# Kernel optimization log

Measured on AMD Instinct MI355X. Metric: run time of the kernel, lower is better.

The kernel has to match this reference:

```python
import jax, jax.numpy as jnp
import numpy as np

B, D, A, K, M = 32768, 64, 32, 16, 128


def _spec(W):
    # SpectralLinear: weight divided by its largest singular value
    s = jnp.linalg.norm(W, ord=2)
    return W / (s + 1e-6)


def setup_inputs() -> dict:
    key = jax.random.key(0)
    ks = jax.random.split(key, 20)

    def rn(i, shape):
        return jax.random.normal(ks[i], shape, jnp.float32) / np.float32(np.sqrt(shape[0]))

    return {
        "z": jax.random.normal(ks[0], (B, D), jnp.float32),
        "action": jax.random.normal(ks[1], (B, A), jnp.float32),
        "rw": jax.random.uniform(ks[2], (B, K), jnp.float32),
        "control": jax.random.normal(ks[3], (B, D), jnp.float32),
        # ActionTokenizer(action_dim, d_model, latent_dim) params (act / control / chart)
        "act_Wx": rn(4, (A + D, M)), "act_bx": jnp.zeros((M,), jnp.float32), "act_Wz": rn(5, (A, D)),
        "ctl_Wx": rn(6, (2 * D, M)), "ctl_bx": jnp.zeros((M,), jnp.float32), "ctl_Wz": rn(7, (D, D)),
        "cht_Wx": rn(8, (K + D, M)), "cht_bx": jnp.zeros((M,), jnp.float32), "cht_Wz": rn(9, (K, D)),
        # z_embed
        "We": rn(10, (D, M)), "be": jnp.zeros((M,), jnp.float32),
        # CovariantAttention (n_heads=1)
        "Wq": rn(11, (M, M)), "Wk": rn(12, (M, M)), "Wv": rn(13, (M, M)), "Wo": rn(14, (M, M)),
        # Spectral output heads
        "cons_W": rn(15, (M, 1)), "cons_b": jnp.zeros((1,), jnp.float32),
        "form_W": rn(16, (M, D)), "form_b": jnp.zeros((D,), jnp.float32),
    }


def reference(z, action, rw, control,
              act_Wx, act_bx, act_Wz,
              ctl_Wx, ctl_bx, ctl_Wz,
              cht_Wx, cht_bx, cht_Wz,
              We, be, Wq, Wk, Wv, Wo,
              cons_W, cons_b, form_W, form_b):
    def tok(u, Wx, bx, Wz):
        # tokenizer: feature token in d_model + associated latent position token
        x = jnp.tanh(jnp.concatenate([u, z], axis=-1) @ Wx + bx)   # [B, M]
        zt = z + jnp.tanh(u @ Wz)                                   # [B, D]
        return x, zt

    act_x, act_z = tok(action, act_Wx, act_bx, act_Wz)
    ctl_x, ctl_z = tok(control, ctl_Wx, ctl_bx, ctl_Wz)
    cht_x, cht_z = tok(rw, cht_Wx, cht_bx, cht_Wz)

    ctx_x = jnp.stack([act_x, ctl_x, cht_x], axis=1)  # [B, 3, M]
    ctx_z = jnp.stack([act_z, ctl_z, cht_z], axis=1)  # [B, 3, D]

    x_q = z @ We + be                                  # [B, M]

    # CovariantAttention: dot-product scores with metric-aware (geodesic distance) bias
    q = x_q @ Wq                                       # [B, M]
    k = ctx_x @ Wk                                     # [B, 3, M]
    v = ctx_x @ Wv                                     # [B, 3, M]
    dist2 = jnp.sum((z[:, None, :] - ctx_z) ** 2, axis=-1)          # [B, 3]
    scores = jnp.einsum('bm,btm->bt', q, k) / np.float32(np.sqrt(M)) - dist2
    attn = jax.nn.softmax(scores, axis=-1)             # [B, 3]
    feat = jnp.einsum('bt,btm->bm', attn, v) @ Wo      # [B, M]

    # Spectral output heads
    reward_conservative = feat @ _spec(cons_W) + cons_b            # [B, 1]
    reward_form_cov = feat @ _spec(form_W) + form_b                # [B, D]
    reward_nonconservative = jnp.sum(reward_form_cov * control, axis=-1, keepdims=True)

    return reward_conservative + reward_nonconservative            # [B, 1]
```

## Files before the change

### kernel.cpp

```cpp
#include <hip/hip_runtime.h>
#include <hip/hip_bf16.h>


typedef float f32x4 __attribute__((ext_vector_type(4)));
typedef short s16x8 __attribute__((ext_vector_type(8)));

#define OFF_ACTX  0
#define OFF_CTLX  24
#define OFF_CHTX  56
#define OFF_ACTZ  80
#define OFF_CTLZ  84
#define OFF_CHTZ  92
#define OFF_WEQK  96
#define OFF_WVOFT 112
#define N_TILES   128
#define SIG_OFF   (N_TILES*1024)
#define PREP_OFF  (SIG_OFF + 256)

__device__ __forceinline__ unsigned short f2bf(float f){
  unsigned u = __float_as_uint(f);
  u += 0x7fffu + ((u>>16)&1u);
  return (unsigned short)(u>>16);
}

__device__ __forceinline__ unsigned cvtpk(float lo, float hi){
  unsigned r;
  asm("v_cvt_pk_bf16_f32 %0, %1, %2" : "=v"(r) : "v"(lo), "v"(hi));
  return r;
}

union V8 { s16x8 v; unsigned short us[8]; uint4 q; };

__device__ __forceinline__ f32x4 MF(s16x8 a, s16x8 b, f32x4 c){
  return __builtin_amdgcn_mfma_f32_16x16x32_bf16(a, b, c, 0, 0, 0);
}

__device__ __forceinline__ s16x8 ldB(const unsigned short* pk, int tile, int lane){
  V8 t;
  t.q = *reinterpret_cast<const uint4*>(pk + ((tile<<6) + lane)*8);
  return t.v;
}

__device__ __forceinline__ s16x8 ldA_g(const float* __restrict__ p, int ko, int limit){
  V8 t;
  if (ko < limit){
    const float4* q4 = reinterpret_cast<const float4*>(p + ko);
    float4 a = q4[0], b = q4[1];
    t.q = make_uint4(cvtpk(a.x,a.y), cvtpk(a.z,a.w), cvtpk(b.x,b.y), cvtpk(b.z,b.w));
  } else {
    t.q = make_uint4(0u,0u,0u,0u);
  }
  return t.v;
}

__device__ __forceinline__ float tanh_fast(float x){
  float e = __expf(2.f*x);
  return 1.f - 2.f*__builtin_amdgcn_rcpf(e + 1.f);
}

__global__ __launch_bounds__(256) void prep_all(
    const float* __restrict__ We, const float* __restrict__ be,
    const float* __restrict__ Wq, const float* __restrict__ Wk,
    const float* __restrict__ Wv, const float* __restrict__ Wo,
    const float* __restrict__ consW, const float* __restrict__ formW,
    const float* __restrict__ aWx, const float* __restrict__ cWx,
    const float* __restrict__ hWx, const float* __restrict__ aWz,
    const float* __restrict__ cWz, const float* __restrict__ hWz,
    unsigned short* __restrict__ packed, float* __restrict__ prep,
    float* __restrict__ sig)
{
  const int b = blockIdx.x;
  const int tid = threadIdx.x;

  if (b < 130){
    __shared__ float Msh[128][129];
    __shared__ float Msh2[128][129];
    __shared__ float tsh[128];
    __shared__ float ph[2][128];
    const int half = tid >> 7, t128 = tid & 127;
    const int m0 = half*64;
    if (b <= 64){
      for (int i4 = tid; i4 < 4096; i4 += 256){
        float4 v = ((const float4*)Wk)[i4];
        int r = i4 >> 5, c = (i4 & 31) << 2;
        Msh[r][c] = v.x; Msh[r][c+1] = v.y; Msh[r][c+2] = v.z; Msh[r][c+3] = v.w;
      }
      const float* rowv = (b == 64) ? be : (We + (size_t)b*128);
      {
        float s = 0.f;
        for (int m = m0; m < m0+64; ++m) s += rowv[m]*Wq[(size_t)m*128 + t128];
        ph[half][t128] = s;
      }
      __syncthreads();
      if (tid < 128) tsh[tid] = ph[0][tid] + ph[1][tid];
      __syncthreads();
      {
        float s1 = 0.f;
        for (int p = m0; p < m0+64; ++p) s1 += tsh[p]*Msh[t128][p];
        ph[half][t128] = s1;
      }
      __syncthreads();
      if (tid < 128){
        float s1 = ph[0][tid] + ph[1][tid];
        if (b == 64) prep[16384 + tid] = s1;
        else {
          int r = b;
          int T = OFF_WEQK + ((r>>5)<<3) + (tid>>4);
          int l2 = (((r&31)>>3)<<4) | (tid&15);
          packed[((size_t)T*64 + l2)*8 + (r&7)] = f2bf(s1);
        }
      }
    } else {
      int d = b - 65;
      for (int i4 = tid; i4 < 4096; i4 += 256){
        float4 v = ((const float4*)Wo)[i4];
        int r = i4 >> 5, c = (i4 & 31) << 2;
        Msh[r][c] = v.x; Msh[r][c+1] = v.y; Msh[r][c+2] = v.z; Msh[r][c+3] = v.w;
      }
      for (int i4 = tid; i4 < 4096; i4 += 256){
        float4 v = ((const float4*)Wv)[i4];
        int r = i4 >> 5, c = (i4 & 31) << 2;
        Msh2[r][c] = v.x; Msh2[r][c+1] = v.y; Msh2[r][c+2] = v.z; Msh2[r][c+3] = v.w;
      }
      __syncthreads();
      {
        float s = 0.f;
        if (d < 64){ for (int j = m0; j < m0+64; ++j) s += Msh[t128][j]*formW[(size_t)j*64 + d]; }
        else       { for (int j = m0; j < m0+64; ++j) s += Msh[t128][j]*consW[j]; }
        ph[half][t128] = s;
      }
      __syncthreads();
      if (tid < 128) tsh[tid] = ph[0][tid] + ph[1][tid];
      __syncthreads();
      {
        float s1 = 0.f;
        for (int p = m0; p < m0+64; ++p) s1 += Msh2[t128][p]*tsh[p];
        ph[half][t128] = s1;
      }
      __syncthreads();
      if (tid < 128){
        float s1 = ph[0][tid] + ph[1][tid];
        if (d < 64){
          int r = d;
          int T = OFF_WVOFT + ((r>>5)<<3) + (tid>>4);
          int l2 = (((r&31)>>3)<<4) | (tid&15);
          packed[((size_t)T*64 + l2)*8 + (r&7)] = f2bf(s1);
        } else prep[16512 + tid] = s1;
      }
    }
    return;
  }

  if (b == 130){
    __shared__ unsigned short SW[8192];
    __shared__ unsigned short SG[4096];

    #pragma unroll
    for (int s4 = 0; s4 < 4; ++s4){
      int q = tid*4 + s4;
      int T = q >> 6, l = q & 63;
      V8 t;
      #pragma unroll
      for (int i = 0; i < 8; ++i){
        int k = (T>>2)*32 + ((l>>4)<<3) + i;
        int n = ((T&3)<<4) + (l&15);
        t.us[i] = f2bf(formW[(size_t)k*64 + n]);
      }
      *reinterpret_cast<uint4*>(&SW[q*8]) = t.q;
    }
    __syncthreads();
    if (tid >= 64) return;
    const int l = tid;
    const f32x4 z4 = {0.f,0.f,0.f,0.f};

    float cs;
    { float c0 = consW[l], c1 = consW[l+64];
      cs = c0*c0 + c1*c1;
      #pragma unroll
      for (int m = 1; m < 64; m <<= 1) cs += __shfl_xor(cs, m);
    }

    s16x8 wf[4][4];
    #pragma unroll
    for (int kt = 0; kt < 4; ++kt)
      #pragma unroll
      for (int x = 0; x < 4; ++x)
        wf[kt][x] = *reinterpret_cast<const s16x8*>(&SW[((((kt<<2)+x)<<6) | l)*8]);

    f32x4 D[4][4];
    #pragma unroll
    for (int it = 0; it < 4; ++it)
      #pragma unroll
      for (int nt = 0; nt < 4; ++nt){
        f32x4 a = z4;
        #pragma unroll
        for (int kt = 0; kt < 4; ++kt) a = MF(wf[kt][it], wf[kt][nt], a);
        D[it][nt] = a;
      }

    float L;
    {
      float ss = 0.f;
      #pragma unroll
      for (int it = 0; it < 4; ++it)
        #pragma unroll
        for (int nt = 0; nt < 4; ++nt)
          #pragma unroll
          for (int j = 0; j < 4; ++j) ss += D[it][nt][j]*D[it][nt][j];
      #pragma unroll
      for (int m = 1; m < 64; m <<= 1) ss += __shfl_xor(ss, m);
      float n0 = sqrtf(ss);
      L = logf(n0);
      float iv = 1.f/n0;
      #pragma unroll
      for (int it = 0; it < 4; ++it){
        int rb2 = it*16 + ((l>>4)<<2);
        int lp  = (((rb2&31)>>3)<<4) | (l&15);
        int ib  = rb2 & 7;
        int ktg = rb2 >> 5;
        #pragma unroll
        for (int nt = 0; nt < 4; ++nt){
          unsigned w0 = (unsigned)f2bf(D[it][nt][0]*iv) | ((unsigned)f2bf(D[it][nt][1]*iv)<<16);
          unsigned w1 = (unsigned)f2bf(D[it][nt][2]*iv) | ((unsigned)f2bf(D[it][nt][3]*iv)<<16);
          uint2 u; u.x = w0; u.y = w1;
          *reinterpret_cast<uint2*>(&SG[((((ktg<<2)+nt)<<6 | lp))*8 + ib]) = u;
        }
      }
    }

    for (int s = 1; s <= 6; ++s){
      s16x8 gf[2][4];
      #pragma unroll
      for (int kt = 0; kt < 2; ++kt)
        #pragma unroll
        for (int x = 0; x < 4; ++x)
          gf[kt][x] = *reinterpret_cast<const s16x8*>(&SG[((((kt<<2)+x)<<6) | l)*8]);
      f32x4 E[4][4];
      #pragma unroll
      for (int it = 0; it < 4; ++it)
        #pragma unroll
        for (int nt = 0; nt < 4; ++nt){
          f32x4 a = MF(gf[0][it], gf[0][nt], z4);
          E[it][nt] = MF(gf[1][it], gf[1][nt], a);
        }
      float ss = 0.f;
      #pragma unroll
      for (int it = 0; it < 4; ++it)
        #pragma unroll
        for (int nt = 0; nt < 4; ++nt)
          #pragma unroll
          for (int j = 0; j < 4; ++j) ss += E[it][nt][j]*E[it][nt][j];
      #pragma unroll
      for (int m = 1; m < 64; m <<= 1) ss += __shfl_xor(ss, m);
      float ns = sqrtf(ss);
      L = 2.f*L + logf(ns);
      if (s < 6){
        float iv = 1.f/ns;
        #pragma unroll
        for (int it = 0; it < 4; ++it){
          int rb2 = it*16 + ((l>>4)<<2);
          int lp  = (((rb2&31)>>3)<<4) | (l&15);
          int ib  = rb2 & 7;
          int ktg = rb2 >> 5;
          #pragma unroll
          for (int nt = 0; nt < 4; ++nt){
            unsigned w0 = (unsigned)f2bf(E[it][nt][0]*iv) | ((unsigned)f2bf(E[it][nt][1]*iv)<<16);
            unsigned w1 = (unsigned)f2bf(E[it][nt][2]*iv) | ((unsigned)f2bf(E[it][nt][3]*iv)<<16);
            uint2 u; u.x = w0; u.y = w1;
            *reinterpret_cast<uint2*>(&SG[((((ktg<<2)+nt)<<6 | lp))*8 + ib]) = u;
          }
        }
      }
    }

    if (l == 0){
      float sf = expf(L*(1.f/128.f));
      sig[0] = 1.f/(sf + 1e-6f);
      sig[1] = 1.f/(sqrtf(cs) + 1e-6f);
    }
    return;
  }

  {
    int tile = b - 131;
    const float* W; int N; int kind = 0; int base;
    if      (tile < 24) { W=aWx; N=128; base=OFF_ACTX; }
    else if (tile < 56) { W=cWx; N=128; base=OFF_CTLX; }
    else if (tile < 80) { W=hWx; N=128; base=OFF_CHTX; kind=1; }
    else if (tile < 84) { W=aWz; N=64;  base=OFF_ACTZ; }
    else if (tile < 92) { W=cWz; N=64;  base=OFF_CTLZ; }
    else                { W=hWz; N=64;  base=OFF_CHTZ; kind=2; }
    int NT = N >> 4;
    int lt = tile - base;
    int nt = lt % NT, kt = lt / NT;
    int l = tid >> 2, i0 = (tid & 3)*2;
    unsigned short us2[2];
    #pragma unroll
    for (int di = 0; di < 2; ++di){
      int i = i0 + di;
      int k = kt*32 + ((l>>4)<<3) + i;
      int n = nt*16 + (l & 15);
      int sr = k;
      if (kind == 1) sr = (k < 16) ? k : (k < 32 ? -1 : k - 16);
      else if (kind == 2) sr = (k < 16) ? k : -1;
      float v = (sr >= 0) ? W[(size_t)sr*N + n] : 0.f;
      us2[di] = f2bf(v);
    }
    *reinterpret_cast<unsigned*>(&packed[((size_t)tile*64 + l)*8 + i0]) =
        (unsigned)us2[0] | ((unsigned)us2[1] << 16);
  }
}

template<int KTX, int KTZ>
__device__ __forceinline__ void token_dot2(
    const unsigned short* pk, int offX, const s16x8 (*afX)[2],
    int offZ, const s16x8 (*afZ)[2], const float* __restrict__ bx,
    int lane, int ntb, int nzb,
    const f32x4 qw[2][4], const f32x4 hw[2][4],
    float st[2][4], float hs[2][4])
{
  const int r15 = lane & 15;
  const f32x4 z4 = {0.f,0.f,0.f,0.f};
  f32x4 acc[2][4];
  #pragma unroll
  for (int s = 0; s < 2; ++s)
    #pragma unroll
    for (int nl = 0; nl < 4; ++nl) acc[s][nl] = z4;
  #pragma unroll
  for (int kt = 0; kt < KTX; ++kt){
    #pragma unroll
    for (int nl = 0; nl < 4; ++nl){
      s16x8 bfr = ldB(pk, offX + kt*8 + ntb + nl, lane);
      acc[0][nl] = MF(afX[kt][0], bfr, acc[0][nl]);
      acc[1][nl] = MF(afX[kt][1], bfr, acc[1][nl]);
    }
  }
  float qs[2][4], hp[2][4];
  #pragma unroll
  for (int s = 0; s < 2; ++s)
    #pragma unroll
    for (int j = 0; j < 4; ++j){ qs[s][j] = 0.f; hp[s][j] = 0.f; }
  #pragma unroll
  for (int nl = 0; nl < 4; ++nl){
    float bv = bx[(ntb + nl)*16 + r15];
    #pragma unroll
    for (int s = 0; s < 2; ++s)
      #pragma unroll
      for (int j = 0; j < 4; ++j){
        float x = tanh_fast(acc[s][nl][j] + bv);
        qs[s][j] += x*qw[s][nl][j];
        hp[s][j] += x*hw[s][nl][j];
      }
  }
  f32x4 a2[2][2];
  #pragma unroll
  for (int s = 0; s < 2; ++s){ a2[s][0] = z4; a2[s][1] = z4; }
  #pragma unroll
  for (int kt = 0; kt < KTZ; ++kt){
    #pragma unroll
    for (int nl = 0; nl < 2; ++nl){
      s16x8 bfr = ldB(pk, offZ + kt*4 + nzb + nl, lane);
      a2[0][nl] = MF(afZ[kt][0], bfr, a2[0][nl]);
      a2[1][nl] = MF(afZ[kt][1], bfr, a2[1][nl]);
    }
  }
  const float isq = 0.0883883476483184f;
  #pragma unroll
  for (int s = 0; s < 2; ++s)
    #pragma unroll
    for (int j = 0; j < 4; ++j){
      float t0 = tanh_fast(a2[s][0][j]);
      float t1 = tanh_fast(a2[s][1][j]);
      st[s][j] = qs[s][j]*isq - (t0*t0 + t1*t1);
      hs[s][j] = hp[s][j];
    }
}

__global__ __launch_bounds__(512, 2) void reward_main(
    const float* __restrict__ z, const float* __restrict__ action,
    const float* __restrict__ rw, const float* __restrict__ control,
    const float* __restrict__ act_bx, const float* __restrict__ ctl_bx,
    const float* __restrict__ cht_bx, const float* __restrict__ consb,
    const float* __restrict__ formb,
    const unsigned short* __restrict__ packed, const float* __restrict__ prep,
    const float* __restrict__ sig, float* __restrict__ out)
{
  __shared__ unsigned short pk_sh[65536];
  __shared__ float ex[128][49];

  const int tid  = threadIdx.x;
  const int wid  = tid >> 6;
  const int lane = tid & 63;
  const int rg   = wid & 3;
  const int mh   = wid >> 2;
  const int g0   = blockIdx.x*128 + rg*32;
  const int r15  = lane & 15;
  const int hi   = lane >> 4;
  const int ko   = hi << 3;
  const int rb   = hi << 2;
  const int ntb  = mh << 2;
  const int nzb  = mh << 1;
  const f32x4 z4 = {0.f,0.f,0.f,0.f};

  {
    auto* gsrc = (const __attribute__((address_space(1))) char*)packed;
    auto* ldst = (__attribute__((address_space(3))) char*)pk_sh;
    #pragma unroll
    for (int it = 0; it < 16; ++it){
      int off = it*8192 + wid*1024;
      __builtin_amdgcn_global_load_lds(
        (const __attribute__((address_space(1))) unsigned*)(gsrc + off + lane*16),
        (__attribute__((address_space(3))) unsigned*)(ldst + off),
        16, 0, 0);
    }
  }

  s16x8 fz0[2], fz1[2], fac[2], fc0[2], fc1[2], frw[2];
  #pragma unroll
  for (int s = 0; s < 2; ++s){
    const int ar = g0 + s*16 + r15;
    fz0[s] = ldA_g(z + (size_t)ar*64,            ko, 64);
    fz1[s] = ldA_g(z + (size_t)ar*64 + 32,       ko, 32);
    fac[s] = ldA_g(action + (size_t)ar*32,       ko, 32);
    fc0[s] = ldA_g(control + (size_t)ar*64,      ko, 64);
    fc1[s] = ldA_g(control + (size_t)ar*64 + 32, ko, 32);
    frw[s] = ldA_g(rw + (size_t)ar*16,           ko, 16);
  }

  if (mh == 0){
    #pragma unroll
    for (int s = 0; s < 2; ++s){
      const int ar = g0 + s*16 + r15;
      const float* cp = control + (size_t)ar*64;
      float4 c0a = *(const float4*)(cp + ko);
      float4 c0b = *(const float4*)(cp + ko + 4);
      float4 c1a = *(const float4*)(cp + 32 + ko);
      float4 c1b = *(const float4*)(cp + 32 + ko + 4);
      float4 f0a = *(const float4*)(formb + ko);
      float4 f0b = *(const float4*)(formb + ko + 4);
      float4 f1a = *(const float4*)(formb + 32 + ko);
      float4 f1b = *(const float4*)(formb + 32 + ko + 4);
      float fbp = c0a.x*f0a.x + c0a.y*f0a.y + c0a.z*f0a.z + c0a.w*f0a.w
                + c0b.x*f0b.x + c0b.y*f0b.y + c0b.z*f0b.z + c0b.w*f0b.w
                + c1a.x*f1a.x + c1a.y*f1a.y + c1a.z*f1a.z + c1a.w*f1a.w
                + c1b.x*f1b.x + c1b.y*f1b.y + c1b.z*f1b.z + c1b.w*f1b.w;
      fbp += __shfl_xor(fbp, 16);
      fbp += __shfl_xor(fbp, 32);
      if (lane < 16) ex[rg*32 + s*16 + r15][48] = fbp;
    }
  }

  const float inv_f = sig[0], inv_c = sig[1];

  __syncthreads();
  const unsigned short* pk = pk_sh;

  f32x4 qw[2][4];
  {
    #pragma unroll
    for (int s = 0; s < 2; ++s)
      #pragma unroll
      for (int nl = 0; nl < 4; ++nl) qw[s][nl] = z4;
    #pragma unroll
    for (int kt = 0; kt < 2; ++kt){
      #pragma unroll
      for (int nl = 0; nl < 4; ++nl){
        s16x8 bfr = ldB(pk, OFF_WEQK + kt*8 + ntb + nl, lane);
        qw[0][nl] = MF(kt == 0 ? fz0[0] : fz1[0], bfr, qw[0][nl]);
        qw[1][nl] = MF(kt == 0 ? fz0[1] : fz1[1], bfr, qw[1][nl]);
      }
    }
    const float* bqk = prep + 16384;
    #pragma unroll
    for (int nl = 0; nl < 4; ++nl){
      float bv = bqk[(ntb + nl)*16 + r15];
      #pragma unroll
      for (int s = 0; s < 2; ++s)
        #pragma unroll
        for (int j = 0; j < 4; ++j) qw[s][nl][j] += bv;
    }
  }

  f32x4 hw[2][4];
  {
    #pragma unroll
    for (int s = 0; s < 2; ++s)
      #pragma unroll
      for (int nl = 0; nl < 4; ++nl) hw[s][nl] = z4;
    #pragma unroll
    for (int kt = 0; kt < 2; ++kt){
      #pragma unroll
      for (int nl = 0; nl < 4; ++nl){
        s16x8 bfr = ldB(pk, OFF_WVOFT + kt*8 + ntb + nl, lane);
        hw[0][nl] = MF(kt == 0 ? fc0[0] : fc1[0], bfr, hw[0][nl]);
        hw[1][nl] = MF(kt == 0 ? fc0[1] : fc1[1], bfr, hw[1][nl]);
      }
    }
    const float* wvoc = prep + 16512;
    #pragma unroll
    for (int nl = 0; nl < 4; ++nl){
      float wvc = inv_c*wvoc[(ntb + nl)*16 + r15];
      #pragma unroll
      for (int s = 0; s < 2; ++s)
        #pragma unroll
        for (int j = 0; j < 4; ++j) hw[s][nl][j] = wvc + inv_f*hw[s][nl][j];
    }
  }

  float st[3][2][4], hs[3][2][4];
  {
    s16x8 afA[3][2] = {{fac[0],fac[1]},{fz0[0],fz0[1]},{fz1[0],fz1[1]}};
    s16x8 afAz[1][2] = {{fac[0],fac[1]}};
    token_dot2<3,1>(pk, OFF_ACTX, afA, OFF_ACTZ, afAz, act_bx, lane, ntb, nzb, qw, hw, st[0], hs[0]);
  }
  {
    s16x8 afC[4][2] = {{fc0[0],fc0[1]},{fc1[0],fc1[1]},{fz0[0],fz0[1]},{fz1[0],fz1[1]}};
    s16x8 afCz[2][2] = {{fc0[0],fc0[1]},{fc1[0],fc1[1]}};
    token_dot2<4,2>(pk, OFF_CTLX, afC, OFF_CTLZ, afCz, ctl_bx, lane, ntb, nzb, qw, hw, st[1], hs[1]);
  }
  {
    s16x8 afH[3][2] = {{frw[0],frw[1]},{fz0[0],fz0[1]},{fz1[0],fz1[1]}};
    s16x8 afHz[1][2] = {{frw[0],frw[1]}};
    token_dot2<3,1>(pk, OFF_CHTX, afH, OFF_CHTZ, afHz, cht_bx, lane, ntb, nzb, qw, hw, st[2], hs[2]);
  }

  #pragma unroll
  for (int m = 1; m < 4; m <<= 1)
    #pragma unroll
    for (int t = 0; t < 3; ++t)
      #pragma unroll
      for (int s = 0; s < 2; ++s)
        #pragma unroll
        for (int j = 0; j < 4; ++j){
          st[t][s][j] += __shfl_xor(st[t][s][j], m);
          hs[t][s][j] += __shfl_xor(hs[t][s][j], m);
        }
  if ((r15 & 3) == 0){
    int gi = r15 >> 2;
    #pragma unroll
    for (int s = 0; s < 2; ++s)
      #pragma unroll
      for (int t = 0; t < 3; ++t)
        #pragma unroll
        for (int j = 0; j < 4; ++j){
          int row = rg*32 + s*16 + rb + j;
          ex[row][t*8 + mh*4 + gi]      = st[t][s][j];
          ex[row][24 + t*8 + mh*4 + gi] = hs[t][s][j];
        }
  }
  __syncthreads();

  if (tid < 128){
    const int row = tid;
    float sv[3], hv[3];
    #pragma unroll
    for (int t = 0; t < 3; ++t){
      float a = 0.f, h = 0.f;
      #pragma unroll
      for (int i = 0; i < 8; ++i){
        a += ex[row][t*8 + i];
        h += ex[row][24 + t*8 + i];
      }
      sv[t] = a; hv[t] = h;
    }
    float mx = fmaxf(sv[0], fmaxf(sv[1], sv[2]));
    float e0 = __expf(sv[0]-mx), e1 = __expf(sv[1]-mx), e2 = __expf(sv[2]-mx);
    float inv = __builtin_amdgcn_rcpf(e0 + e1 + e2);
    float tot = (e0*hv[0] + e1*hv[1] + e2*hv[2])*inv + ex[row][48] + consb[0];
    out[blockIdx.x*128 + row] = tot;
  }
}

extern "C" void kernel_launch(void* const* d_in, const int* in_sizes, int n_in,
                              void* d_out, int out_size, void* d_ws, size_t ws_size,
                              hipStream_t stream)
{
  const float* z      = (const float*)d_in[0];
  const float* action = (const float*)d_in[1];
  const float* rw     = (const float*)d_in[2];
  const float* control= (const float*)d_in[3];
  const float* actWx  = (const float*)d_in[4];
  const float* actbx  = (const float*)d_in[5];
  const float* actWz  = (const float*)d_in[6];
  const float* ctlWx  = (const float*)d_in[7];
  const float* ctlbx  = (const float*)d_in[8];
  const float* ctlWz  = (const float*)d_in[9];
  const float* chtWx  = (const float*)d_in[10];
  const float* chtbx  = (const float*)d_in[11];
  const float* chtWz  = (const float*)d_in[12];
  const float* We     = (const float*)d_in[13];
  const float* be     = (const float*)d_in[14];
  const float* Wq     = (const float*)d_in[15];
  const float* Wk     = (const float*)d_in[16];
  const float* Wv     = (const float*)d_in[17];
  const float* Wo     = (const float*)d_in[18];
  const float* consW  = (const float*)d_in[19];
  const float* consb  = (const float*)d_in[20];
  const float* formW  = (const float*)d_in[21];
  const float* formb  = (const float*)d_in[22];
  float* out = (float*)d_out;

  unsigned short* packed = (unsigned short*)d_ws;
  float* sig  = (float*)((char*)d_ws + SIG_OFF);
  float* prep = (float*)((char*)d_ws + PREP_OFF);

  hipLaunchKernelGGL(prep_all, dim3(227), dim3(256), 0, stream,
                     We, be, Wq, Wk, Wv, Wo, consW, formW,
                     actWx, ctlWx, chtWx, actWz, ctlWz, chtWz,
                     packed, prep, sig);
  hipLaunchKernelGGL(reward_main, dim3(256), dim3(512), 0, stream,
                     z, action, rw, control, actbx, ctlbx, chtbx,
                     consb, formb, packed, prep, sig, out);
}
```

Before: 33.12 us.

## Stream packed weights through double-buffered LDS chunks instead of full preload

Replaces the 128KB whole-weight LDS preload with a 2x8KB double buffer. Each 8KB chunk is staged with global_load_lds while the previous chunk feeds MFMAs, with a block barrier per chunk. The much smaller LDS footprint lets launch bounds ask for 4 blocks per CU instead of 2, and the shuffle reduction and exchange layout are reworked to match. The cost is many more __syncthreads and repeated weight fetches from L2 by every block, and the per-chunk stage is not visibly waited on before use.

```diff
diff --git a/kernel.cpp b/kernel.cpp
--- a/kernel.cpp
+++ b/kernel.cpp
@@ -35,9 +35,9 @@
   return __builtin_amdgcn_mfma_f32_16x16x32_bf16(a, b, c, 0, 0, 0);
 }
 
-__device__ __forceinline__ s16x8 ldB(const unsigned short* pk, int tile, int lane){
+__device__ __forceinline__ s16x8 ldBc(const unsigned short* buf, int tl, int lane){
   V8 t;
-  t.q = *reinterpret_cast<const uint4*>(pk + ((tile<<6) + lane)*8);
+  t.q = *reinterpret_cast<const uint4*>(buf + (tl*64 + lane)*8);
   return t.v;
 }
 
@@ -56,6 +56,57 @@
 __device__ __forceinline__ float tanh_fast(float x){
   float e = __expf(2.f*x);
   return 1.f - 2.f*__builtin_amdgcn_rcpf(e + 1.f);
+}
+
+__device__ __forceinline__ void xch(const unsigned short* buf, int ntb, int lane,
+                                    s16x8 a0, s16x8 a1, f32x4 (&acc)[2][4]){
+  #pragma unroll
+  for (int nl = 0; nl < 4; ++nl){
+    s16x8 bfr = ldBc(buf, ntb + nl, lane);
+    acc[0][nl] = MF(a0, bfr, acc[0][nl]);
+    acc[1][nl] = MF(a1, bfr, acc[1][nl]);
+  }
+}
+
+__device__ __forceinline__ void zch(const unsigned short* buf, int tlo, int nzb, int lane,
+                                    s16x8 a0, s16x8 a1, f32x4 (&az)[2][2]){
+  #pragma unroll
+  for (int nl = 0; nl < 2; ++nl){
+    s16x8 bfr = ldBc(buf, tlo + nzb + nl, lane);
+    az[0][nl] = MF(a0, bfr, az[0][nl]);
+    az[1][nl] = MF(a1, bfr, az[1][nl]);
+  }
+}
+
+__device__ __forceinline__ void fin_tok(const f32x4 (&acc)[2][4], const float* bxv,
+                                        const f32x4 (&qw)[2][4], const f32x4 (&hw)[2][4],
+                                        float (&stt)[2][4], float (&hst)[2][4]){
+  const float isq = 0.0883883476483184f;
+  #pragma unroll
+  for (int s = 0; s < 2; ++s)
+    #pragma unroll
+    for (int j = 0; j < 4; ++j){
+      float qs = 0.f, hp = 0.f;
+      #pragma unroll
+      for (int nl = 0; nl < 4; ++nl){
+        float x = tanh_fast(acc[s][nl][j] + bxv[nl]);
+        qs += x*qw[s][nl][j];
+        hp += x*hw[s][nl][j];
+      }
+      stt[s][j] = qs*isq;
+      hst[s][j] = hp;
+    }
+}
+
+__device__ __forceinline__ void d2_fin(const f32x4 (&az)[2][2], float (&stt)[2][4]){
+  #pragma unroll
+  for (int s = 0; s < 2; ++s)
+    #pragma unroll
+    for (int j = 0; j < 4; ++j){
+      float t0 = tanh_fast(az[s][0][j]);
+      float t1 = tanh_fast(az[s][1][j]);
+      stt[s][j] -= (t0*t0 + t1*t1);
+    }
 }
 
 __global__ __launch_bounds__(256) void prep_all(
@@ -311,72 +362,7 @@
   }
 }
 
-template<int KTX, int KTZ>
-__device__ __forceinline__ void token_dot2(
-    const unsigned short* pk, int offX, const s16x8 (*afX)[2],
-    int offZ, const s16x8 (*afZ)[2], const float* __restrict__ bx,
-    int lane, int ntb, int nzb,
-    const f32x4 qw[2][4], const f32x4 hw[2][4],
-    float st[2][4], float hs[2][4])
-{
-  const int r15 = lane & 15;
-  const f32x4 z4 = {0.f,0.f,0.f,0.f};
-  f32x4 acc[2][4];
-  #pragma unroll
-  for (int s = 0; s < 2; ++s)
-    #pragma unroll
-    for (int nl = 0; nl < 4; ++nl) acc[s][nl] = z4;
-  #pragma unroll
-  for (int kt = 0; kt < KTX; ++kt){
-    #pragma unroll
-    for (int nl = 0; nl < 4; ++nl){
-      s16x8 bfr = ldB(pk, offX + kt*8 + ntb + nl, lane);
-      acc[0][nl] = MF(afX[kt][0], bfr, acc[0][nl]);
-      acc[1][nl] = MF(afX[kt][1], bfr, acc[1][nl]);
-    }
-  }
-  float qs[2][4], hp[2][4];
-  #pragma unroll
-  for (int s = 0; s < 2; ++s)
-    #pragma unroll
-    for (int j = 0; j < 4; ++j){ qs[s][j] = 0.f; hp[s][j] = 0.f; }
-  #pragma unroll
-  for (int nl = 0; nl < 4; ++nl){
-    float bv = bx[(ntb + nl)*16 + r15];
-    #pragma unroll
-    for (int s = 0; s < 2; ++s)
-      #pragma unroll
-      for (int j = 0; j < 4; ++j){
-        float x = tanh_fast(acc[s][nl][j] + bv);
-        qs[s][j] += x*qw[s][nl][j];
-        hp[s][j] += x*hw[s][nl][j];
-      }
-  }
-  f32x4 a2[2][2];
-  #pragma unroll
-  for (int s = 0; s < 2; ++s){ a2[s][0] = z4; a2[s][1] = z4; }
-  #pragma unroll
-  for (int kt = 0; kt < KTZ; ++kt){
-    #pragma unroll
-    for (int nl = 0; nl < 2; ++nl){
-      s16x8 bfr = ldB(pk, offZ + kt*4 + nzb + nl, lane);
-      a2[0][nl] = MF(afZ[kt][0], bfr, a2[0][nl]);
-      a2[1][nl] = MF(afZ[kt][1], bfr, a2[1][nl]);
-    }
-  }
-  const float isq = 0.0883883476483184f;
-  #pragma unroll
-  for (int s = 0; s < 2; ++s)
-    #pragma unroll
-    for (int j = 0; j < 4; ++j){
-      float t0 = tanh_fast(a2[s][0][j]);
-      float t1 = tanh_fast(a2[s][1][j]);
-      st[s][j] = qs[s][j]*isq - (t0*t0 + t1*t1);
-      hs[s][j] = hp[s][j];
-    }
-}
-
-__global__ __launch_bounds__(512, 2) void reward_main(
+__global__ __launch_bounds__(512, 4) void reward_main(
     const float* __restrict__ z, const float* __restrict__ action,
     const float* __restrict__ rw, const float* __restrict__ control,
     const float* __restrict__ act_bx, const float* __restrict__ ctl_bx,
@@ -385,8 +371,8 @@
     const unsigned short* __restrict__ packed, const float* __restrict__ prep,
     const float* __restrict__ sig, float* __restrict__ out)
 {
-  __shared__ unsigned short pk_sh[65536];
-  __shared__ float ex[128][49];
+  __shared__ __align__(16) unsigned short bufs[2][4096];
+  __shared__ float ex[128][25];
 
   const int tid  = threadIdx.x;
   const int wid  = tid >> 6;
@@ -402,18 +388,16 @@
   const int nzb  = mh << 1;
   const f32x4 z4 = {0.f,0.f,0.f,0.f};
 
-  {
+  auto STAGE = [&](int chunk, int par){
     auto* gsrc = (const __attribute__((address_space(1))) char*)packed;
-    auto* ldst = (__attribute__((address_space(3))) char*)pk_sh;
-    #pragma unroll
-    for (int it = 0; it < 16; ++it){
-      int off = it*8192 + wid*1024;
-      __builtin_amdgcn_global_load_lds(
-        (const __attribute__((address_space(1))) unsigned*)(gsrc + off + lane*16),
-        (__attribute__((address_space(3))) unsigned*)(ldst + off),
-        16, 0, 0);
-    }
-  }
+    auto* ldst = (__attribute__((address_space(3))) char*)(&bufs[par][0]);
+    __builtin_amdgcn_global_load_lds(
+      (const __attribute__((address_space(1))) unsigned*)(gsrc + chunk*8192 + wid*1024 + lane*16),
+      (__attribute__((address_space(3))) unsigned*)(ldst + wid*1024),
+      16, 0, 0);
+  };
+
+  STAGE(12, 0);
 
   s16x8 fz0[2], fz1[2], fac[2], fc0[2], fc1[2], frw[2];
   #pragma unroll
@@ -426,6 +410,19 @@
     fc1[s] = ldA_g(control + (size_t)ar*64 + 32, ko, 32);
     frw[s] = ldA_g(rw + (size_t)ar*16,           ko, 16);
   }
+
+  float bxA[4], bxC[4], bxH[4], bqkv[4], wvocv[4];
+  {
+    const float* bqk  = prep + 16384;
+    const float* wvoc = prep + 16512;
+    #pragma unroll
+    for (int nl = 0; nl < 4; ++nl){
+      int idx = (ntb + nl)*16 + r15;
+      bxA[nl] = act_bx[idx]; bxC[nl] = ctl_bx[idx]; bxH[nl] = cht_bx[idx];
+      bqkv[nl] = bqk[idx];   wvocv[nl] = wvoc[idx];
+    }
+  }
+  const float inv_f = sig[0], inv_c = sig[1];
 
   if (mh == 0){
     #pragma unroll
@@ -446,86 +443,120 @@
                 + c1b.x*f1b.x + c1b.y*f1b.y + c1b.z*f1b.z + c1b.w*f1b.w;
       fbp += __shfl_xor(fbp, 16);
       fbp += __shfl_xor(fbp, 32);
-      if (lane < 16) ex[rg*32 + s*16 + r15][48] = fbp;
-    }
-  }
-
-  const float inv_f = sig[0], inv_c = sig[1];
-
-  __syncthreads();
-  const unsigned short* pk = pk_sh;
+      if (lane < 16) ex[rg*32 + s*16 + r15][24] = fbp;
+    }
+  }
+  __syncthreads();
 
   f32x4 qw[2][4];
-  {
+  #pragma unroll
+  for (int s = 0; s < 2; ++s)
+    #pragma unroll
+    for (int nl = 0; nl < 4; ++nl) qw[s][nl] = z4;
+  STAGE(13, 1);
+  xch(bufs[0], ntb, lane, fz0[0], fz0[1], qw);
+  __syncthreads();
+
+  STAGE(14, 0);
+  xch(bufs[1], ntb, lane, fz1[0], fz1[1], qw);
+  #pragma unroll
+  for (int nl = 0; nl < 4; ++nl)
     #pragma unroll
     for (int s = 0; s < 2; ++s)
       #pragma unroll
-      for (int nl = 0; nl < 4; ++nl) qw[s][nl] = z4;
-    #pragma unroll
-    for (int kt = 0; kt < 2; ++kt){
-      #pragma unroll
-      for (int nl = 0; nl < 4; ++nl){
-        s16x8 bfr = ldB(pk, OFF_WEQK + kt*8 + ntb + nl, lane);
-        qw[0][nl] = MF(kt == 0 ? fz0[0] : fz1[0], bfr, qw[0][nl]);
-        qw[1][nl] = MF(kt == 0 ? fz0[1] : fz1[1], bfr, qw[1][nl]);
-      }
-    }
-    const float* bqk = prep + 16384;
-    #pragma unroll
-    for (int nl = 0; nl < 4; ++nl){
-      float bv = bqk[(ntb + nl)*16 + r15];
-      #pragma unroll
-      for (int s = 0; s < 2; ++s)
-        #pragma unroll
-        for (int j = 0; j < 4; ++j) qw[s][nl][j] += bv;
-    }
-  }
+      for (int j = 0; j < 4; ++j) qw[s][nl][j] += bqkv[nl];
+  __syncthreads();
 
   f32x4 hw[2][4];
-  {
+  #pragma unroll
+  for (int s = 0; s < 2; ++s)
+    #pragma unroll
+    for (int nl = 0; nl < 4; ++nl) hw[s][nl] = z4;
+  STAGE(15, 1);
+  xch(bufs[0], ntb, lane, fc0[0], fc0[1], hw);
+  __syncthreads();
+
+  STAGE(0, 0);
+  xch(bufs[1], ntb, lane, fc1[0], fc1[1], hw);
+  #pragma unroll
+  for (int nl = 0; nl < 4; ++nl){
+    float wvc = inv_c*wvocv[nl];
     #pragma unroll
     for (int s = 0; s < 2; ++s)
       #pragma unroll
-      for (int nl = 0; nl < 4; ++nl) hw[s][nl] = z4;
-    #pragma unroll
-    for (int kt = 0; kt < 2; ++kt){
-      #pragma unroll
-      for (int nl = 0; nl < 4; ++nl){
-        s16x8 bfr = ldB(pk, OFF_WVOFT + kt*8 + ntb + nl, lane);
-        hw[0][nl] = MF(kt == 0 ? fc0[0] : fc1[0], bfr, hw[0][nl]);
-        hw[1][nl] = MF(kt == 0 ? fc0[1] : fc1[1], bfr, hw[1][nl]);
-      }
-    }
-    const float* wvoc = prep + 16512;
-    #pragma unroll
-    for (int nl = 0; nl < 4; ++nl){
-      float wvc = inv_c*wvoc[(ntb + nl)*16 + r15];
-      #pragma unroll
-      for (int s = 0; s < 2; ++s)
-        #pragma unroll
-        for (int j = 0; j < 4; ++j) hw[s][nl][j] = wvc + inv_f*hw[s][nl][j];
-    }
-  }
+      for (int j = 0; j < 4; ++j) hw[s][nl][j] = wvc + inv_f*hw[s][nl][j];
+  }
+  __syncthreads();
 
   float st[3][2][4], hs[3][2][4];
-  {
-    s16x8 afA[3][2] = {{fac[0],fac[1]},{fz0[0],fz0[1]},{fz1[0],fz1[1]}};
-    s16x8 afAz[1][2] = {{fac[0],fac[1]}};
-    token_dot2<3,1>(pk, OFF_ACTX, afA, OFF_ACTZ, afAz, act_bx, lane, ntb, nzb, qw, hw, st[0], hs[0]);
-  }
-  {
-    s16x8 afC[4][2] = {{fc0[0],fc0[1]},{fc1[0],fc1[1]},{fz0[0],fz0[1]},{fz1[0],fz1[1]}};
-    s16x8 afCz[2][2] = {{fc0[0],fc0[1]},{fc1[0],fc1[1]}};
-    token_dot2<4,2>(pk, OFF_CTLX, afC, OFF_CTLZ, afCz, ctl_bx, lane, ntb, nzb, qw, hw, st[1], hs[1]);
-  }
-  {
-    s16x8 afH[3][2] = {{frw[0],frw[1]},{fz0[0],fz0[1]},{fz1[0],fz1[1]}};
-    s16x8 afHz[1][2] = {{frw[0],frw[1]}};
-    token_dot2<3,1>(pk, OFF_CHTX, afH, OFF_CHTZ, afHz, cht_bx, lane, ntb, nzb, qw, hw, st[2], hs[2]);
-  }
-
-  #pragma unroll
-  for (int m = 1; m < 4; m <<= 1)
+  f32x4 accX[2][4];
+
+  #pragma unroll
+  for (int s = 0; s < 2; ++s)
+    #pragma unroll
+    for (int nl = 0; nl < 4; ++nl) accX[s][nl] = z4;
+  STAGE(1, 1);
+  xch(bufs[0], ntb, lane, fac[0], fac[1], accX);
+  __syncthreads();
+  STAGE(2, 0);
+  xch(bufs[1], ntb, lane, fz0[0], fz0[1], accX);
+  __syncthreads();
+  STAGE(3, 1);
+  xch(bufs[0], ntb, lane, fz1[0], fz1[1], accX);
+  fin_tok(accX, bxA, qw, hw, st[0], hs[0]);
+  __syncthreads();
+
+  #pragma unroll
+  for (int s = 0; s < 2; ++s)
+    #pragma unroll
+    for (int nl = 0; nl < 4; ++nl) accX[s][nl] = z4;
+  STAGE(4, 0);
+  xch(bufs[1], ntb, lane, fc0[0], fc0[1], accX);
+  __syncthreads();
+  STAGE(5, 1);
+  xch(bufs[0], ntb, lane, fc1[0], fc1[1], accX);
+  __syncthreads();
+  STAGE(6, 0);
+  xch(bufs[1], ntb, lane, fz0[0], fz0[1], accX);
+  __syncthreads();
+  STAGE(7, 1);
+  xch(bufs[0], ntb, lane, fz1[0], fz1[1], accX);
+  fin_tok(accX, bxC, qw, hw, st[1], hs[1]);
+  __syncthreads();
+
+  #pragma unroll
+  for (int s = 0; s < 2; ++s)
+    #pragma unroll
+    for (int nl = 0; nl < 4; ++nl) accX[s][nl] = z4;
+  STAGE(8, 0);
+  xch(bufs[1], ntb, lane, frw[0], frw[1], accX);
+  __syncthreads();
+  STAGE(9, 1);
+  xch(bufs[0], ntb, lane, fz0[0], fz0[1], accX);
+  __syncthreads();
+  STAGE(10, 0);
+  xch(bufs[1], ntb, lane, fz1[0], fz1[1], accX);
+  fin_tok(accX, bxH, qw, hw, st[2], hs[2]);
+  __syncthreads();
+
+  f32x4 a2T[2][2], a2C[2][2];
+  #pragma unroll
+  for (int s = 0; s < 2; ++s){ a2T[s][0]=z4; a2T[s][1]=z4; a2C[s][0]=z4; a2C[s][1]=z4; }
+  STAGE(11, 1);
+  zch(bufs[0], 0, nzb, lane, fac[0], fac[1], a2T);
+  zch(bufs[0], 4, nzb, lane, fc0[0], fc0[1], a2C);
+  d2_fin(a2T, st[0]);
+  __syncthreads();
+
+  zch(bufs[1], 0, nzb, lane, fc1[0], fc1[1], a2C);
+  #pragma unroll
+  for (int s = 0; s < 2; ++s){ a2T[s][0]=z4; a2T[s][1]=z4; }
+  zch(bufs[1], 4, nzb, lane, frw[0], frw[1], a2T);
+  d2_fin(a2C, st[1]);
+  d2_fin(a2T, st[2]);
+
+  #pragma unroll
+  for (int m = 1; m < 8; m <<= 1)
     #pragma unroll
     for (int t = 0; t < 3; ++t)
       #pragma unroll
@@ -535,8 +566,8 @@
           st[t][s][j] += __shfl_xor(st[t][s][j], m);
           hs[t][s][j] += __shfl_xor(hs[t][s][j], m);
         }
-  if ((r15 & 3) == 0){
-    int gi = r15 >> 2;
+  if ((r15 & 7) == 0){
+    int gi = r15 >> 3;
     #pragma unroll
     for (int s = 0; s < 2; ++s)
       #pragma unroll
@@ -544,8 +575,8 @@
         #pragma unroll
         for (int j = 0; j < 4; ++j){
           int row = rg*32 + s*16 + rb + j;
-          ex[row][t*8 + mh*4 + gi]      = st[t][s][j];
-          ex[row][24 + t*8 + mh*4 + gi] = hs[t][s][j];
+          ex[row][t*4 + mh*2 + gi]      = st[t][s][j];
+          ex[row][12 + t*4 + mh*2 + gi] = hs[t][s][j];
         }
   }
   __syncthreads();
@@ -557,16 +588,16 @@
     for (int t = 0; t < 3; ++t){
       float a = 0.f, h = 0.f;
       #pragma unroll
-      for (int i = 0; i < 8; ++i){
-        a += ex[row][t*8 + i];
-        h += ex[row][24 + t*8 + i];
+      for (int i = 0; i < 4; ++i){
+        a += ex[row][t*4 + i];
+        h += ex[row][12 + t*4 + i];
       }
       sv[t] = a; hv[t] = h;
     }
     float mx = fmaxf(sv[0], fmaxf(sv[1], sv[2]));
     float e0 = __expf(sv[0]-mx), e1 = __expf(sv[1]-mx), e2 = __expf(sv[2]-mx);
     float inv = __builtin_amdgcn_rcpf(e0 + e1 + e2);
-    float tot = (e0*hv[0] + e1*hv[1] + e2*hv[2])*inv + ex[row][48] + consb[0];
+    float tot = (e0*hv[0] + e1*hv[1] + e2*hv[2])*inv + ex[row][24] + consb[0];
     out[blockIdx.x*128 + row] = tot;
   }
 }
```

New measurement: 57.51 us. +73.6%, slower.
